# Optimization experiments

Measured on AMD Instinct MI355X. Metric: run time of the kernel, lower is better.

## Reference

```python
import jax, jax.numpy as jnp
import numpy as np
import math

B, N, D, H, O = 2, 1024, 256, 4, 8
DT, STEPS = 0.1, 5


def setup_inputs() -> dict:
    key = jax.random.key(0)
    ks = jax.random.split(key, 8)
    inv_d = 1.0 / math.sqrt(D)
    inv_ho = 1.0 / math.sqrt(H * O)
    return {
        "x": jax.random.normal(ks[0], (B, N, D), jnp.float32),
        "Wq": jax.random.normal(ks[1], (D, D), jnp.float32) * inv_d,
        "Wk": jax.random.normal(ks[2], (D, D), jnp.float32) * inv_d,
        "Wp": jax.random.normal(ks[3], (H * O, D), jnp.float32) * inv_d,
        "bp": jnp.zeros((H * O,), jnp.float32),
        "Wo": jax.random.normal(ks[4], (D, H * O), jnp.float32) * inv_ho,
        "bo": jnp.zeros((D,), jnp.float32),
        "omega": jax.random.normal(ks[5], (H, O), jnp.float32) * 0.1,
        "coupling_scale": jnp.asarray(1.0, jnp.float32),
    }


def reference(x, Wq, Wk, Wp, bp, Wo, bo, omega, coupling_scale):
    dk = D // H
    # attention coupling J_ij = softmax(q_i.k_j / sqrt(d_k))  -> (B,H,N,N)
    q = (x @ Wq.T).reshape(B, N, H, dk).transpose(0, 2, 1, 3)
    k = (x @ Wk.T).reshape(B, N, H, dk).transpose(0, 2, 1, 3)
    J = jax.nn.softmax(jnp.einsum('bhid,bhjd->bhij', q, k) / math.sqrt(dk), axis=-1)
    # initial phases (B,H,N,O)
    phases = (x @ Wp.T + bp).reshape(B, N, H, O).transpose(0, 2, 1, 3)
    om = omega[None, :, None, :]  # (1,H,1,O)

    def step(ph, _):
        # sum_j J_ij sin(phi_j - phi_i) = cos(phi_i)*(J@sin phi) - sin(phi_i)*(J@cos phi)
        s, c = jnp.sin(ph), jnp.cos(ph)
        coupling = c * jnp.einsum('bhij,bhjo->bhio', J, s) - s * jnp.einsum('bhij,bhjo->bhio', J, c)
        new = ph + DT * (om + coupling_scale * coupling)
        new = jnp.remainder(new + jnp.pi, 2 * jnp.pi) - jnp.pi
        return new, None

    phases, _ = jax.lax.scan(step, phases, None, length=STEPS)
    sig = jnp.cos(phases).transpose(0, 2, 1, 3).reshape(B, N, H * O)
    return sig @ Wo.T + bo
```

## Files before the change

kernel.cpp:

```cpp
#include <hip/hip_runtime.h>
#include <hip/hip_bf16.h>
#include <math.h>


#define NB 1024
#define NH 4
#define DD 256
#define NO 8
#define SCSZ 131072
#define PI_F      3.14159265358979323846f
#define TWO_PI_F  6.28318530717958647692f
#define INV_2PI_F 0.15915494309189533577f

typedef __attribute__((ext_vector_type(8))) short bf16x8;
typedef __attribute__((ext_vector_type(4))) float f32x4;
typedef unsigned long long u64;

__device__ __forceinline__ float b2f_u(unsigned short s) {
    union { unsigned u; float f; } x; x.u = ((unsigned)s) << 16; return x.f;
}
__device__ __forceinline__ unsigned short f2b(float f) {
    union { float f; unsigned u; } v; v.f = f;
    unsigned r = v.u + 0x7FFFu + ((v.u >> 16) & 1u);
    return (unsigned short)(r >> 16);
}
template<bool F32>
__device__ __forceinline__ uint4 load_pack8(const void* p, size_t off) {
    if (!F32) return *(const uint4*)((const unsigned short*)p + off);
    const float* fp = (const float*)p + off;
    float4 a = *(const float4*)fp;
    float4 b = *(const float4*)(fp + 4);
    uint4 r;
    r.x = (unsigned)f2b(a.x) | ((unsigned)f2b(a.y) << 16);
    r.y = (unsigned)f2b(a.z) | ((unsigned)f2b(a.w) << 16);
    r.z = (unsigned)f2b(b.x) | ((unsigned)f2b(b.y) << 16);
    r.w = (unsigned)f2b(b.z) | ((unsigned)f2b(b.w) << 16);
    return r;
}
__device__ __forceinline__ void load8_rt(int f32, const void* p, int i, float* f) {
    if (f32) {
        const float* fp = (const float*)p + i;
        float4 a = *(const float4*)fp;
        float4 b = *(const float4*)(fp + 4);
        f[0]=a.x; f[1]=a.y; f[2]=a.z; f[3]=a.w;
        f[4]=b.x; f[5]=b.y; f[6]=b.z; f[7]=b.w;
    } else {
        uint4 u = *(const uint4*)((const unsigned short*)p + i);
        f[0] = b2f_u(u.x & 0xFFFFu); f[1] = b2f_u(u.x >> 16);
        f[2] = b2f_u(u.y & 0xFFFFu); f[3] = b2f_u(u.y >> 16);
        f[4] = b2f_u(u.z & 0xFFFFu); f[5] = b2f_u(u.z >> 16);
        f[6] = b2f_u(u.w & 0xFFFFu); f[7] = b2f_u(u.w >> 16);
    }
}
__device__ __forceinline__ float read_cs_bf16(const void* p) {
    float vb = b2f_u(*(const unsigned short*)p);
    bool ok = isfinite(vb) && fabsf(vb) > 1e-30f && fabsf(vb) < 1e30f;
    if (ok) return vb;
    return *(const float*)p;
}
__device__ __forceinline__ int detect_inline(const unsigned short* x) {
    int l = threadIdx.x & 63;
    float a0 = fabsf(b2f_u(x[2 * l]));
    float a1 = fabsf(b2f_u(x[2 * (l + 64)]));
    unsigned long long b0 = __ballot(!(a0 >= 1e-10f && a0 <= 100.0f));
    unsigned long long b1 = __ballot(!(a1 >= 1e-10f && a1 <= 100.0f));
    return (__popcll(b0) + __popcll(b1)) > 16;
}
__device__ __forceinline__ void st8_llc(void* p, u64 v) {
    __hip_atomic_store((u64*)p, v, __ATOMIC_RELAXED, __HIP_MEMORY_SCOPE_AGENT);
}
__device__ __forceinline__ void st4_llc(unsigned* p, unsigned v) {
    __hip_atomic_store(p, v, __ATOMIC_RELAXED, __HIP_MEMORY_SCOPE_AGENT);
}
__device__ __forceinline__ void wait_flags64(const unsigned* f, unsigned tgt) {
    const int l = threadIdx.x & 63;
    unsigned spins = 0;
    for (;;) {
        unsigned v = __hip_atomic_load(f + l, __ATOMIC_RELAXED,
                                       __HIP_MEMORY_SCOPE_AGENT);
        if (__all((int)(v >= tgt))) break;
        __builtin_amdgcn_s_sleep(1);
        if (++spins > (1u << 18)) break;
    }
}

template<bool F32>
__device__ void projm_impl(
    const void* __restrict__ x, const void* __restrict__ Wq,
    const void* __restrict__ Wk, const void* __restrict__ Wp,
    const void* __restrict__ bp,
    unsigned short* __restrict__ Qb, unsigned short* __restrict__ Kb,
    float* __restrict__ PH, unsigned short* __restrict__ SC)
{
    __shared__ uint4 Xsh[64 * 32];
    __shared__ uint4 Wsh[64 * 32];
    const int tid = threadIdx.x;
    const int ftile = blockIdx.x % 9, itile = blockIdx.x / 9;
    const int i0 = itile * 64, f0 = ftile * 64;
    const int wave = tid >> 6, lane = tid & 63;
    const int n = lane & 15, quad = lane >> 4;

    #pragma unroll
    for (int g = 0; g < 8; g++) {
        int fidx = g * 256 + tid;
        int row = fidx >> 5, q = fidx & 31;
        int sw = (q & 24) | ((q ^ row) & 7);
        Xsh[row * 32 + sw] = load_pack8<F32>(x, (size_t)(i0 + row) * 256 + q * 8);
        int wr = f0 + row;
        uint4 wv = make_uint4(0, 0, 0, 0);
        if (wr < 256)      wv = load_pack8<F32>(Wq, (size_t)wr * 256 + q * 8);
        else if (wr < 512) wv = load_pack8<F32>(Wk, (size_t)(wr - 256) * 256 + q * 8);
        else if (wr < 544) wv = load_pack8<F32>(Wp, (size_t)(wr - 512) * 256 + q * 8);
        Wsh[row * 32 + sw] = wv;
    }
    __syncthreads();

    f32x4 acc[4];
    #pragma unroll
    for (int s = 0; s < 4; s++) acc[s] = (f32x4){0.f, 0.f, 0.f, 0.f};
    const int xrow = wave * 16 + n;
    #pragma unroll
    for (int s = 0; s < 8; s++) {
        int qc = s * 4 + quad;
        bf16x8 b = ((const bf16x8*)Xsh)[xrow * 32 + ((qc & 24) | ((qc ^ xrow) & 7))];
        #pragma unroll
        for (int sub = 0; sub < 4; sub++) {
            int wr = sub * 16 + n;
            bf16x8 a = ((const bf16x8*)Wsh)[wr * 32 + ((qc & 24) | ((qc ^ wr) & 7))];
            acc[sub] = __builtin_amdgcn_mfma_f32_16x16x32_bf16(a, b, acc[sub], 0, 0, 0);
        }
    }

    const int ig = i0 + wave * 16 + n;
    const int bb = ig >> 10, nr = ig & 1023;
    if (ftile < 4) {
        #pragma unroll
        for (int sub = 0; sub < 4; sub++) {
            int dd = sub * 16 + quad * 4;
            ushort4 v = make_ushort4(f2b(acc[sub][0] * 0.125f), f2b(acc[sub][1] * 0.125f),
                                     f2b(acc[sub][2] * 0.125f), f2b(acc[sub][3] * 0.125f));
            *(ushort4*)(Qb + ((size_t)((bb * NH + ftile) * NB + nr)) * 64 + dd) = v;
        }
    } else if (ftile < 8) {
        int h = ftile - 4;
        #pragma unroll
        for (int sub = 0; sub < 4; sub++) {
            int dd = sub * 16 + quad * 4;
            ushort4 v = make_ushort4(f2b(acc[sub][0]), f2b(acc[sub][1]),
                                     f2b(acc[sub][2]), f2b(acc[sub][3]));
            *(ushort4*)(Kb + ((size_t)((bb * NH + h) * NB + nr)) * 64 + dd) = v;
        }
    } else {
        #pragma unroll
        for (int sub = 0; sub < 2; sub++) {
            #pragma unroll
            for (int r = 0; r < 4; r++) {
                int fp = sub * 16 + quad * 4 + r;
                int h2 = fp >> 3, o = fp & 7;
                float bpv = F32 ? ((const float*)bp)[fp]
                                : b2f_u(((const unsigned short*)bp)[fp]);
                float v = acc[sub][r] + bpv;
                int bh = bb * NH + h2;
                PH[(size_t)bh * 8192 + o * 1024 + nr] = v;
                float sv, cv;
                __sincosf(v, &sv, &cv);
                SC[(size_t)(bh * 16 + o) * 1024 + nr]     = f2b(sv);
                SC[(size_t)(bh * 16 + 8 + o) * 1024 + nr] = f2b(cv);
            }
        }
    }
}

__global__ __launch_bounds__(256) void k_projm(
    const unsigned short* x, const void* Wq, const void* Wk, const void* Wp,
    const void* bp, unsigned short* Qb, unsigned short* Kb, float* PH,
    unsigned short* SC, unsigned int* flg)
{
    if (blockIdx.x == 0) {
        flg[threadIdx.x] = 0u;
        flg[threadIdx.x + 256] = 0u;
    }
    if (detect_inline(x)) projm_impl<true >(x, Wq, Wk, Wp, bp, Qb, Kb, PH, SC);
    else                  projm_impl<false>(x, Wq, Wk, Wp, bp, Qb, Kb, PH, SC);
}

__global__ __launch_bounds__(256) void k_mega4(
    const unsigned short* __restrict__ xraw,
    const unsigned short* __restrict__ Qb, const unsigned short* __restrict__ Kb,
    const float* __restrict__ PH0,
    unsigned short* __restrict__ SCB,
    const void* __restrict__ omega, const void* __restrict__ csp,
    const void* __restrict__ Wo, const void* __restrict__ bo,
    void* __restrict__ out, unsigned int* __restrict__ flg)
{
    __shared__ uint4 Ush[16 * 128];
    __shared__ f32x4 red[4][64];
    __shared__ float redS[4][16];
    __shared__ float Rsh[16];
    __shared__ float sig[4][32];

    const int tid = threadIdx.x;
    const int bid = blockIdx.x;
    const int bh    = bid & 7;
    const int chunk = bid >> 3;
    const int cid   = bh * 64 + chunk;
    const int i0    = chunk * 16;
    const int wave = tid >> 6, lane = tid & 63;
    const int n = lane & 15, quad = lane >> 4;
    const int f32 = detect_inline(xraw);

    const unsigned short* qrow = Qb + ((size_t)(bh * NB) + i0 + n) * 64;
    bf16x8 bq0 = *(const bf16x8*)(qrow + quad * 8);
    bf16x8 bq1 = *(const bf16x8*)(qrow + 32 + quad * 8);
    float s = 0.f;
    const unsigned short* kbase = Kb + ((size_t)(bh * NB) + n) * 64;
    #pragma unroll
    for (int t = 0; t < 16; t++) {
        int jt = wave * 16 + t;
        const unsigned short* arow = kbase + (size_t)jt * 16 * 64;
        bf16x8 a0 = *(const bf16x8*)(arow + quad * 8);
        bf16x8 a1 = *(const bf16x8*)(arow + 32 + quad * 8);
        f32x4 acc = {0.f, 0.f, 0.f, 0.f};
        acc = __builtin_amdgcn_mfma_f32_16x16x32_bf16(a0, bq0, acc, 0, 0, 0);
        acc = __builtin_amdgcn_mfma_f32_16x16x32_bf16(a1, bq1, acc, 0, 0, 0);
        float u0 = __expf(acc[0]);
        float u1 = __expf(acc[1]);
        float u2 = __expf(acc[2]);
        float u3 = __expf(acc[3]);
        s += (u0 + u1) + (u2 + u3);
        ushort4 uv = make_ushort4(f2b(u0), f2b(u1), f2b(u2), f2b(u3));
        int cw = 2 * jt + (quad >> 1);
        ((ushort4*)Ush)[(n * 128 + (cw ^ (n & 7))) * 2 + (quad & 1)] = uv;
    }
    s += __shfl_xor(s, 16);
    s += __shfl_xor(s, 32);
    if (lane < 16) redS[wave][lane] = s;
    __syncthreads();
    if (tid < 16)
        Rsh[tid] = 1.0f / (redS[0][tid] + redS[1][tid] + redS[2][tid] + redS[3][tid]);

    float P[4];
    float cs_ = 0.f, om_ = 0.f;
    if (wave == 0 && n < 8) {
        const int o = n, h = bh & 3;
        cs_ = f32 ? *(const float*)csp : read_cs_bf16(csp);
        om_ = f32 ? ((const float*)omega)[h * NO + o]
                  : b2f_u(((const unsigned short*)omega)[h * NO + o]);
        float4 pv = *(const float4*)(PH0 + (size_t)bh * 8192 + o * 1024 + i0 + quad * 4);
        P[0] = pv.x; P[1] = pv.y; P[2] = pv.z; P[3] = pv.w;
    }

    #pragma unroll 1
    for (int k = 0; k < 5; k++) {
        const unsigned short* scrow = SCB + (size_t)k * SCSZ + (size_t)(bh * 16 + n) * 1024;
        unsigned short* scout       = SCB + (size_t)(k + 1) * SCSZ;
        f32x4 acc = {0.f, 0.f, 0.f, 0.f};
        #pragma unroll
        for (int t = 0; t < 8; t++) {
            int it = wave * 8 + t;
            bf16x8 a = ((const bf16x8*)Ush)[n * 128 + ((it * 4 + quad) ^ (n & 7))];
            bf16x8 b = *(const bf16x8*)(scrow + it * 32 + quad * 8);
            acc = __builtin_amdgcn_mfma_f32_16x16x32_bf16(a, b, acc, 0, 0, 0);
        }
        red[wave][lane] = acc;
        __syncthreads();

        if (wave == 0) {
            f32x4 a0 = red[0][lane], a1 = red[1][lane];
            f32x4 a2 = red[2][lane], a3 = red[3][lane];
            #pragma unroll
            for (int v = 0; v < 4; v++) acc[v] = (a0[v] + a1[v]) + (a2[v] + a3[v]);
            float C0 = __shfl_xor(acc[0], 8);
            float C1 = __shfl_xor(acc[1], 8);
            float C2 = __shfl_xor(acc[2], 8);
            float C3 = __shfl_xor(acc[3], 8);
            if (n < 8) {
                const int o = n;
                float S[4] = {acc[0], acc[1], acc[2], acc[3]};
                float C[4] = {C0, C1, C2, C3};
                float Rr[4] = {Rsh[quad * 4], Rsh[quad * 4 + 1],
                               Rsh[quad * 4 + 2], Rsh[quad * 4 + 3]};
                unsigned short sb[4], cb[4];
                #pragma unroll
                for (int r = 0; r < 4; r++) {
                    float si, ci;
                    __sincosf(P[r], &si, &ci);
                    float coup = (ci * S[r] - si * C[r]) * Rr[r];
                    float v = P[r] + 0.1f * (om_ + cs_ * coup);
                    float t2 = v + PI_F;
                    t2 -= floorf(t2 * INV_2PI_F) * TWO_PI_F;
                    P[r] = t2 - PI_F;
                    float sn, cn;
                    __sincosf(P[r], &sn, &cn);
                    sb[r] = f2b(sn); cb[r] = f2b(cn);
                }
                u64 sv = (u64)sb[0] | ((u64)sb[1] << 16) | ((u64)sb[2] << 32) | ((u64)sb[3] << 48);
                u64 cv = (u64)cb[0] | ((u64)cb[1] << 16) | ((u64)cb[2] << 32) | ((u64)cb[3] << 48);
                int i = i0 + quad * 4;
                if (k < 4)
                    st8_llc(scout + (size_t)(bh * 16 + o) * 1024 + i, sv);
                st8_llc(scout + (size_t)(bh * 16 + 8 + o) * 1024 + i, cv);
            }
        }
        __syncthreads();
        if (tid == 0) st4_llc(&flg[cid], (unsigned)(k + 1));
        if (k < 4) {
            if (wave == 0) wait_flags64(flg + bh * 64, (unsigned)(k + 1));
        } else {
            const int ob = bh >> 2;
            const int jc = (chunk >> 2) + 16 * (bh & 3);
            if (wave == 0) {
                unsigned spins = 0;
                for (;;) {
                    int ok = 1;
                    if (lane < 4) {
                        unsigned v = __hip_atomic_load(
                            &flg[(ob * 4 + lane) * 64 + jc],
                            __ATOMIC_RELAXED, __HIP_MEMORY_SCOPE_AGENT);
                        ok = (v >= 5u);
                    }
                    if (__all(ok)) break;
                    __builtin_amdgcn_s_sleep(1);
                    if (++spins > (1u << 18)) break;
                }
            }
        }
        __syncthreads();
    }

    const unsigned short* scfin = SCB + (size_t)5 * SCSZ;
    const int ob = bh >> 2;
    const int n0 = (chunk | ((bh & 3) << 6)) * 4;
    if (tid < 32) {
        int h = tid >> 3, o = tid & 7;
        u64 q = *(const u64*)(scfin + (size_t)((ob * NH + h) * 16 + 8 + o) * 1024 + n0);
        #pragma unroll
        for (int r = 0; r < 4; r++)
            sig[r][tid] = b2f_u((unsigned short)(q >> (16 * r)));
    }
    __syncthreads();
    float wv[32];
    #pragma unroll
    for (int d0 = 0; d0 < 32; d0 += 8) load8_rt(f32, Wo, tid * 32 + d0, wv + d0);
    const float bov = f32 ? ((const float*)bo)[tid] : b2f_u(((const unsigned short*)bo)[tid]);
    #pragma unroll
    for (int r = 0; r < 4; r++) {
        float acc = bov;
        #pragma unroll
        for (int t = 0; t < 32; t++) acc += sig[r][t] * wv[t];
        size_t oi = ((size_t)ob * 1024 + n0 + r) * DD + tid;
        if (f32) ((float*)out)[oi] = acc;
        else     ((unsigned short*)out)[oi] = f2b(acc);
    }
}

extern "C" void kernel_launch(void* const* d_in, const int* in_sizes, int n_in,
                              void* d_out, int out_size, void* d_ws, size_t ws_size,
                              hipStream_t stream)
{
    const unsigned short* x = (const unsigned short*)d_in[0];
    const void* Wq  = d_in[1];
    const void* Wk  = d_in[2];
    const void* Wp  = d_in[3];
    const void* bp  = d_in[4];
    const void* Wo  = d_in[5];
    const void* bo  = d_in[6];
    const void* om  = d_in[7];
    const void* cs  = d_in[8];

    char* w = (char*)d_ws;
    unsigned short* Qb  = (unsigned short*)w;
    unsigned short* Kb  = (unsigned short*)(w + (1u << 20));
    float*          PH0 = (float*)(w + (2u << 20));
    unsigned short* SCB = (unsigned short*)(w + (2u << 20) + (256u << 10));
    unsigned int*   flg = (unsigned int*)(w + (4u << 20));

    k_projm<<<288, 256, 0, stream>>>(x, Wq, Wk, Wp, bp, Qb, Kb, PH0, SCB, flg);
    k_mega4<<<512, 256, 0, stream>>>(x, Qb, Kb, PH0, SCB, om, cs,
                                     Wo, bo, d_out, flg);
}
```

Measured before the change: 119.3 us.

## Fuse projection kernel into the persistent mega kernel with per-block Q/K/phase compute

Removes the separate projection launch. Each of the 512 blocks now computes its own 16-row K tile (written to global), Q tile (kept in shared memory) and initial phases via scalar dot products, then publishes sin/cos and signals a flag before the attention and Kuramoto steps. Flags become 64-bit with a magic high word, and a host memset resets them. This cuts the inter-kernel gap and the Q/PH global round trip, at the cost of redundant weight loads per block and an extra grid-wide barrier before attention.

```diff
diff --git a/kernel.cpp b/kernel.cpp
--- a/kernel.cpp
+++ b/kernel.cpp
@@ -11,6 +11,7 @@
 #define PI_F      3.14159265358979323846f
 #define TWO_PI_F  6.28318530717958647692f
 #define INV_2PI_F 0.15915494309189533577f
+#define MAGIC_HI  0x9E37A5B3u
 
 typedef __attribute__((ext_vector_type(8))) short bf16x8;
 typedef __attribute__((ext_vector_type(4))) float f32x4;
@@ -24,18 +25,19 @@
     unsigned r = v.u + 0x7FFFu + ((v.u >> 16) & 1u);
     return (unsigned short)(r >> 16);
 }
-template<bool F32>
-__device__ __forceinline__ uint4 load_pack8(const void* p, size_t off) {
-    if (!F32) return *(const uint4*)((const unsigned short*)p + off);
-    const float* fp = (const float*)p + off;
-    float4 a = *(const float4*)fp;
-    float4 b = *(const float4*)(fp + 4);
-    uint4 r;
-    r.x = (unsigned)f2b(a.x) | ((unsigned)f2b(a.y) << 16);
-    r.y = (unsigned)f2b(a.z) | ((unsigned)f2b(a.w) << 16);
-    r.z = (unsigned)f2b(b.x) | ((unsigned)f2b(b.y) << 16);
-    r.w = (unsigned)f2b(b.z) | ((unsigned)f2b(b.w) << 16);
-    return r;
+__device__ __forceinline__ uint4 load_pack8_rt(int f32v, const void* p, size_t off) {
+    if (f32v) {
+        const float* fp = (const float*)p + off;
+        float4 a = *(const float4*)fp;
+        float4 b = *(const float4*)(fp + 4);
+        uint4 r;
+        r.x = (unsigned)f2b(a.x) | ((unsigned)f2b(a.y) << 16);
+        r.y = (unsigned)f2b(a.z) | ((unsigned)f2b(a.w) << 16);
+        r.z = (unsigned)f2b(b.x) | ((unsigned)f2b(b.y) << 16);
+        r.w = (unsigned)f2b(b.z) | ((unsigned)f2b(b.w) << 16);
+        return r;
+    }
+    return *(const uint4*)((const unsigned short*)p + off);
 }
 __device__ __forceinline__ void load8_rt(int f32, const void* p, int i, float* f) {
     if (f32) {
@@ -52,6 +54,18 @@
         f[6] = b2f_u(u.w & 0xFFFFu); f[7] = b2f_u(u.w >> 16);
     }
 }
+__device__ __forceinline__ float dot8_bf(uint4 xv, uint4 wv) {
+    float r;
+    r  = b2f_u((unsigned short)(xv.x & 0xFFFFu)) * b2f_u((unsigned short)(wv.x & 0xFFFFu));
+    r += b2f_u((unsigned short)(xv.x >> 16))     * b2f_u((unsigned short)(wv.x >> 16));
+    r += b2f_u((unsigned short)(xv.y & 0xFFFFu)) * b2f_u((unsigned short)(wv.y & 0xFFFFu));
+    r += b2f_u((unsigned short)(xv.y >> 16))     * b2f_u((unsigned short)(wv.y >> 16));
+    r += b2f_u((unsigned short)(xv.z & 0xFFFFu)) * b2f_u((unsigned short)(wv.z & 0xFFFFu));
+    r += b2f_u((unsigned short)(xv.z >> 16))     * b2f_u((unsigned short)(wv.z >> 16));
+    r += b2f_u((unsigned short)(xv.w & 0xFFFFu)) * b2f_u((unsigned short)(wv.w & 0xFFFFu));
+    r += b2f_u((unsigned short)(xv.w >> 16))     * b2f_u((unsigned short)(wv.w >> 16));
+    return r;
+}
 __device__ __forceinline__ float read_cs_bf16(const void* p) {
     float vb = b2f_u(*(const unsigned short*)p);
     bool ok = isfinite(vb) && fabsf(vb) > 1e-30f && fabsf(vb) < 1e30f;
@@ -69,132 +83,34 @@
 __device__ __forceinline__ void st8_llc(void* p, u64 v) {
     __hip_atomic_store((u64*)p, v, __ATOMIC_RELAXED, __HIP_MEMORY_SCOPE_AGENT);
 }
-__device__ __forceinline__ void st4_llc(unsigned* p, unsigned v) {
-    __hip_atomic_store(p, v, __ATOMIC_RELAXED, __HIP_MEMORY_SCOPE_AGENT);
-}
-__device__ __forceinline__ void wait_flags64(const unsigned* f, unsigned tgt) {
+__device__ __forceinline__ void wait_flags_m(const u64* f, unsigned tgt) {
     const int l = threadIdx.x & 63;
     unsigned spins = 0;
     for (;;) {
-        unsigned v = __hip_atomic_load(f + l, __ATOMIC_RELAXED,
-                                       __HIP_MEMORY_SCOPE_AGENT);
-        if (__all((int)(v >= tgt))) break;
+        u64 v = __hip_atomic_load(f + l, __ATOMIC_RELAXED,
+                                  __HIP_MEMORY_SCOPE_AGENT);
+        int ok = ((unsigned)(v >> 32) == MAGIC_HI) && ((unsigned)v >= tgt);
+        if (__all(ok)) break;
         __builtin_amdgcn_s_sleep(1);
         if (++spins > (1u << 18)) break;
     }
 }
 
-template<bool F32>
-__device__ void projm_impl(
-    const void* __restrict__ x, const void* __restrict__ Wq,
-    const void* __restrict__ Wk, const void* __restrict__ Wp,
-    const void* __restrict__ bp,
-    unsigned short* __restrict__ Qb, unsigned short* __restrict__ Kb,
-    float* __restrict__ PH, unsigned short* __restrict__ SC)
-{
-    __shared__ uint4 Xsh[64 * 32];
-    __shared__ uint4 Wsh[64 * 32];
-    const int tid = threadIdx.x;
-    const int ftile = blockIdx.x % 9, itile = blockIdx.x / 9;
-    const int i0 = itile * 64, f0 = ftile * 64;
-    const int wave = tid >> 6, lane = tid & 63;
-    const int n = lane & 15, quad = lane >> 4;
-
-    #pragma unroll
-    for (int g = 0; g < 8; g++) {
-        int fidx = g * 256 + tid;
-        int row = fidx >> 5, q = fidx & 31;
-        int sw = (q & 24) | ((q ^ row) & 7);
-        Xsh[row * 32 + sw] = load_pack8<F32>(x, (size_t)(i0 + row) * 256 + q * 8);
-        int wr = f0 + row;
-        uint4 wv = make_uint4(0, 0, 0, 0);
-        if (wr < 256)      wv = load_pack8<F32>(Wq, (size_t)wr * 256 + q * 8);
-        else if (wr < 512) wv = load_pack8<F32>(Wk, (size_t)(wr - 256) * 256 + q * 8);
-        else if (wr < 544) wv = load_pack8<F32>(Wp, (size_t)(wr - 512) * 256 + q * 8);
-        Wsh[row * 32 + sw] = wv;
-    }
-    __syncthreads();
-
-    f32x4 acc[4];
-    #pragma unroll
-    for (int s = 0; s < 4; s++) acc[s] = (f32x4){0.f, 0.f, 0.f, 0.f};
-    const int xrow = wave * 16 + n;
-    #pragma unroll
-    for (int s = 0; s < 8; s++) {
-        int qc = s * 4 + quad;
-        bf16x8 b = ((const bf16x8*)Xsh)[xrow * 32 + ((qc & 24) | ((qc ^ xrow) & 7))];
-        #pragma unroll
-        for (int sub = 0; sub < 4; sub++) {
-            int wr = sub * 16 + n;
-            bf16x8 a = ((const bf16x8*)Wsh)[wr * 32 + ((qc & 24) | ((qc ^ wr) & 7))];
-            acc[sub] = __builtin_amdgcn_mfma_f32_16x16x32_bf16(a, b, acc[sub], 0, 0, 0);
-        }
-    }
-
-    const int ig = i0 + wave * 16 + n;
-    const int bb = ig >> 10, nr = ig & 1023;
-    if (ftile < 4) {
-        #pragma unroll
-        for (int sub = 0; sub < 4; sub++) {
-            int dd = sub * 16 + quad * 4;
-            ushort4 v = make_ushort4(f2b(acc[sub][0] * 0.125f), f2b(acc[sub][1] * 0.125f),
-                                     f2b(acc[sub][2] * 0.125f), f2b(acc[sub][3] * 0.125f));
-            *(ushort4*)(Qb + ((size_t)((bb * NH + ftile) * NB + nr)) * 64 + dd) = v;
-        }
-    } else if (ftile < 8) {
-        int h = ftile - 4;
-        #pragma unroll
-        for (int sub = 0; sub < 4; sub++) {
-            int dd = sub * 16 + quad * 4;
-            ushort4 v = make_ushort4(f2b(acc[sub][0]), f2b(acc[sub][1]),
-                                     f2b(acc[sub][2]), f2b(acc[sub][3]));
-            *(ushort4*)(Kb + ((size_t)((bb * NH + h) * NB + nr)) * 64 + dd) = v;
-        }
-    } else {
-        #pragma unroll
-        for (int sub = 0; sub < 2; sub++) {
-            #pragma unroll
-            for (int r = 0; r < 4; r++) {
-                int fp = sub * 16 + quad * 4 + r;
-                int h2 = fp >> 3, o = fp & 7;
-                float bpv = F32 ? ((const float*)bp)[fp]
-                                : b2f_u(((const unsigned short*)bp)[fp]);
-                float v = acc[sub][r] + bpv;
-                int bh = bb * NH + h2;
-                PH[(size_t)bh * 8192 + o * 1024 + nr] = v;
-                float sv, cv;
-                __sincosf(v, &sv, &cv);
-                SC[(size_t)(bh * 16 + o) * 1024 + nr]     = f2b(sv);
-                SC[(size_t)(bh * 16 + 8 + o) * 1024 + nr] = f2b(cv);
-            }
-        }
-    }
-}
-
-__global__ __launch_bounds__(256) void k_projm(
-    const unsigned short* x, const void* Wq, const void* Wk, const void* Wp,
-    const void* bp, unsigned short* Qb, unsigned short* Kb, float* PH,
-    unsigned short* SC, unsigned int* flg)
-{
-    if (blockIdx.x == 0) {
-        flg[threadIdx.x] = 0u;
-        flg[threadIdx.x + 256] = 0u;
-    }
-    if (detect_inline(x)) projm_impl<true >(x, Wq, Wk, Wp, bp, Qb, Kb, PH, SC);
-    else                  projm_impl<false>(x, Wq, Wk, Wp, bp, Qb, Kb, PH, SC);
-}
-
-__global__ __launch_bounds__(256) void k_mega4(
+__global__ __launch_bounds__(256) void k_one(
     const unsigned short* __restrict__ xraw,
-    const unsigned short* __restrict__ Qb, const unsigned short* __restrict__ Kb,
-    const float* __restrict__ PH0,
+    const void* __restrict__ Wq, const void* __restrict__ Wk,
+    const void* __restrict__ Wp, const void* __restrict__ bp,
+    unsigned short* __restrict__ Kb,
     unsigned short* __restrict__ SCB,
     const void* __restrict__ omega, const void* __restrict__ csp,
     const void* __restrict__ Wo, const void* __restrict__ bo,
-    void* __restrict__ out, unsigned int* __restrict__ flg)
+    void* __restrict__ out, u64* __restrict__ flg)
 {
     __shared__ uint4 Ush[16 * 128];
     __shared__ f32x4 red[4][64];
+    __shared__ uint4 Xs[16 * 32];
+    __shared__ unsigned short Qs[16 * 64];
+    __shared__ float Psh[8 * 16];
     __shared__ float redS[4][16];
     __shared__ float Rsh[16];
     __shared__ float sig[4][32];
@@ -205,13 +121,119 @@
     const int chunk = bid >> 3;
     const int cid   = bh * 64 + chunk;
     const int i0    = chunk * 16;
+    const int h     = bh & 3;
     const int wave = tid >> 6, lane = tid & 63;
     const int n = lane & 15, quad = lane >> 4;
     const int f32 = detect_inline(xraw);
 
-    const unsigned short* qrow = Qb + ((size_t)(bh * NB) + i0 + n) * 64;
-    bf16x8 bq0 = *(const bf16x8*)(qrow + quad * 8);
-    bf16x8 bq1 = *(const bf16x8*)(qrow + 32 + quad * 8);
+    {
+        const size_t xbase = ((size_t)(bh >> 2) * 1024 + i0) * 256;
+        #pragma unroll
+        for (int g = 0; g < 2; g++) {
+            int fidx = g * 256 + tid;
+            int row = fidx >> 5, q = fidx & 31;
+            Xs[row * 32 + ((q & 24) | ((q ^ row) & 7))] =
+                load_pack8_rt(f32, xraw, xbase + (size_t)row * 256 + q * 8);
+        }
+        #pragma unroll
+        for (int g = 0; g < 8; g++) {
+            int fidx = g * 256 + tid;
+            int row = fidx >> 5, q = fidx & 31;
+            Ush[row * 32 + ((q & 24) | ((q ^ row) & 7))] =
+                load_pack8_rt(f32, Wk, (size_t)(h * 64 + row) * 256 + q * 8);
+        }
+    }
+    __syncthreads();
+
+    {
+        f32x4 ka = {0.f, 0.f, 0.f, 0.f};
+        #pragma unroll
+        for (int s = 0; s < 8; s++) {
+            int qc = s * 4 + quad;
+            bf16x8 bx = ((const bf16x8*)Xs)[n * 32 + ((qc & 24) | ((qc ^ n) & 7))];
+            int wr = wave * 16 + n;
+            bf16x8 aw = ((const bf16x8*)Ush)[wr * 32 + ((qc & 24) | ((qc ^ wr) & 7))];
+            ka = __builtin_amdgcn_mfma_f32_16x16x32_bf16(aw, bx, ka, 0, 0, 0);
+        }
+        u64 kv = (u64)f2b(ka[0]) | ((u64)f2b(ka[1]) << 16)
+               | ((u64)f2b(ka[2]) << 32) | ((u64)f2b(ka[3]) << 48);
+        st8_llc(Kb + ((size_t)(bh * NB) + i0 + n) * 64 + wave * 16 + quad * 4, kv);
+    }
+    __syncthreads();
+
+    {
+        #pragma unroll
+        for (int g = 0; g < 8; g++) {
+            int fidx = g * 256 + tid;
+            int row = fidx >> 5, q = fidx & 31;
+            Ush[row * 32 + ((q & 24) | ((q ^ row) & 7))] =
+                load_pack8_rt(f32, Wq, (size_t)(h * 64 + row) * 256 + q * 8);
+        }
+        uint4* wps = (uint4*)red;
+        int row = tid >> 5, q = tid & 31;
+        wps[row * 32 + q] =
+            load_pack8_rt(f32, Wp, (size_t)(h * 8 + row) * 256 + q * 8);
+    }
+    __syncthreads();
+
+    {
+        f32x4 qa = {0.f, 0.f, 0.f, 0.f};
+        #pragma unroll
+        for (int s = 0; s < 8; s++) {
+            int qc = s * 4 + quad;
+            bf16x8 bx = ((const bf16x8*)Xs)[n * 32 + ((qc & 24) | ((qc ^ n) & 7))];
+            int wr = wave * 16 + n;
+            bf16x8 aw = ((const bf16x8*)Ush)[wr * 32 + ((qc & 24) | ((qc ^ wr) & 7))];
+            qa = __builtin_amdgcn_mfma_f32_16x16x32_bf16(aw, bx, qa, 0, 0, 0);
+        }
+        ushort4 qv = make_ushort4(f2b(qa[0] * 0.125f), f2b(qa[1] * 0.125f),
+                                  f2b(qa[2] * 0.125f), f2b(qa[3] * 0.125f));
+        *(ushort4*)(Qs + n * 64 + wave * 16 + quad * 4) = qv;
+
+        if (tid < 128) {
+            int row = tid >> 3, o = tid & 7;
+            float bpv = f32 ? ((const float*)bp)[h * 8 + o]
+                            : b2f_u(((const unsigned short*)bp)[h * 8 + o]);
+            float accp = bpv;
+            const uint4* wps = (const uint4*)red;
+            #pragma unroll
+            for (int s2 = 0; s2 < 32; s2++) {
+                uint4 xv = Xs[row * 32 + ((s2 & 24) | ((s2 ^ row) & 7))];
+                accp += dot8_bf(xv, wps[o * 32 + s2]);
+            }
+            Psh[o * 16 + row] = accp;
+        }
+    }
+    __syncthreads();
+
+    float P[4];
+    float cs_ = 0.f, om_ = 0.f;
+    if (wave == 0 && n < 8) {
+        const int o = n;
+        cs_ = f32 ? *(const float*)csp : read_cs_bf16(csp);
+        om_ = f32 ? ((const float*)omega)[h * NO + o]
+                  : b2f_u(((const unsigned short*)omega)[h * NO + o]);
+        unsigned short sb[4], cb[4];
+        #pragma unroll
+        for (int r = 0; r < 4; r++) {
+            P[r] = Psh[n * 16 + quad * 4 + r];
+            float sn, cn;
+            __sincosf(P[r], &sn, &cn);
+            sb[r] = f2b(sn); cb[r] = f2b(cn);
+        }
+        u64 sv = (u64)sb[0] | ((u64)sb[1] << 16) | ((u64)sb[2] << 32) | ((u64)sb[3] << 48);
+        u64 cv = (u64)cb[0] | ((u64)cb[1] << 16) | ((u64)cb[2] << 32) | ((u64)cb[3] << 48);
+        int i = i0 + quad * 4;
+        st8_llc(SCB + (size_t)(bh * 16 + o) * 1024 + i,     sv);
+        st8_llc(SCB + (size_t)(bh * 16 + 8 + o) * 1024 + i, cv);
+    }
+    __syncthreads();
+    if (tid == 0) st8_llc(&flg[cid], ((u64)MAGIC_HI << 32) | 1u);
+    if (wave == 0) wait_flags_m(flg + bh * 64, 1u);
+    __syncthreads();
+
+    bf16x8 bq0 = *(const bf16x8*)(Qs + n * 64 + quad * 8);
+    bf16x8 bq1 = *(const bf16x8*)(Qs + n * 64 + 32 + quad * 8);
     float s = 0.f;
     const unsigned short* kbase = Kb + ((size_t)(bh * NB) + n) * 64;
     #pragma unroll
@@ -238,17 +260,6 @@
     __syncthreads();
     if (tid < 16)
         Rsh[tid] = 1.0f / (redS[0][tid] + redS[1][tid] + redS[2][tid] + redS[3][tid]);
-
-    float P[4];
-    float cs_ = 0.f, om_ = 0.f;
-    if (wave == 0 && n < 8) {
-        const int o = n, h = bh & 3;
-        cs_ = f32 ? *(const float*)csp : read_cs_bf16(csp);
-        om_ = f32 ? ((const float*)omega)[h * NO + o]
-                  : b2f_u(((const unsigned short*)omega)[h * NO + o]);
-        float4 pv = *(const float4*)(PH0 + (size_t)bh * 8192 + o * 1024 + i0 + quad * 4);
-        P[0] = pv.x; P[1] = pv.y; P[2] = pv.z; P[3] = pv.w;
-    }
 
     #pragma unroll 1
     for (int k = 0; k < 5; k++) {
@@ -303,9 +314,9 @@
             }
         }
         __syncthreads();
-        if (tid == 0) st4_llc(&flg[cid], (unsigned)(k + 1));
+        if (tid == 0) st8_llc(&flg[cid], ((u64)MAGIC_HI << 32) | (u64)(k + 2));
         if (k < 4) {
-            if (wave == 0) wait_flags64(flg + bh * 64, (unsigned)(k + 1));
+            if (wave == 0) wait_flags_m(flg + bh * 64, (unsigned)(k + 2));
         } else {
             const int ob = bh >> 2;
             const int jc = (chunk >> 2) + 16 * (bh & 3);
@@ -314,10 +325,10 @@
                 for (;;) {
                     int ok = 1;
                     if (lane < 4) {
-                        unsigned v = __hip_atomic_load(
+                        u64 v = __hip_atomic_load(
                             &flg[(ob * 4 + lane) * 64 + jc],
                             __ATOMIC_RELAXED, __HIP_MEMORY_SCOPE_AGENT);
-                        ok = (v >= 5u);
+                        ok = ((unsigned)(v >> 32) == MAGIC_HI) && ((unsigned)v >= 6u);
                     }
                     if (__all(ok)) break;
                     __builtin_amdgcn_s_sleep(1);
@@ -332,8 +343,8 @@
     const int ob = bh >> 2;
     const int n0 = (chunk | ((bh & 3) << 6)) * 4;
     if (tid < 32) {
-        int h = tid >> 3, o = tid & 7;
-        u64 q = *(const u64*)(scfin + (size_t)((ob * NH + h) * 16 + 8 + o) * 1024 + n0);
+        int h2 = tid >> 3, o = tid & 7;
+        u64 q = *(const u64*)(scfin + (size_t)((ob * NH + h2) * 16 + 8 + o) * 1024 + n0);
         #pragma unroll
         for (int r = 0; r < 4; r++)
             sig[r][tid] = b2f_u((unsigned short)(q >> (16 * r)));
@@ -369,13 +380,11 @@
     const void* cs  = d_in[8];
 
     char* w = (char*)d_ws;
-    unsigned short* Qb  = (unsigned short*)w;
     unsigned short* Kb  = (unsigned short*)(w + (1u << 20));
-    float*          PH0 = (float*)(w + (2u << 20));
     unsigned short* SCB = (unsigned short*)(w + (2u << 20) + (256u << 10));
-    unsigned int*   flg = (unsigned int*)(w + (4u << 20));
-
-    k_projm<<<288, 256, 0, stream>>>(x, Wq, Wk, Wp, bp, Qb, Kb, PH0, SCB, flg);
-    k_mega4<<<512, 256, 0, stream>>>(x, Qb, Kb, PH0, SCB, om, cs,
-                                     Wo, bo, d_out, flg);
-}
+    u64*            flg = (u64*)(w + (4u << 20));
+
+    hipMemsetAsync(flg, 0, 512 * sizeof(u64), stream);
+    k_one<<<512, 256, 0, stream>>>(x, Wq, Wk, Wp, bp, Kb, SCB, om, cs,
+                                   Wo, bo, d_out, flg);
+}
```

Result: slower. 123.3 us (+3.4%).
